# Performance work log

Measured on AMD Instinct MI355X. Metric: run time of the kernel, lower is better.

Reference implementation:

```python
import jax, jax.numpy as jnp
import numpy as np

BZ, QL, KL, D = 8, 2048, 2048, 128
SCALE = 1.0 / (D ** 0.5)
NEG = -1000000000.0


def setup_inputs() -> dict:
    key = jax.random.key(0)
    kq, kk, kv, km = jax.random.split(key, 4)
    q = jax.random.normal(kq, (BZ, QL, D), dtype=jnp.float32)
    k = jax.random.normal(kk, (BZ, KL, D), dtype=jnp.float32)
    v = jax.random.normal(kv, (BZ, KL, D), dtype=jnp.float32)
    mask = jax.random.randint(km, (BZ, KL), 0, 2).astype(jnp.bool_)
    return {"q": q, "k": k, "v": v, "mask": mask}


def reference(q, k, v, mask):
    # scores: (bz, q_len, k_len)
    score = jnp.einsum('bqd,bkd->bqk', q, k) * SCALE
    # masked_fill where ~mask (padding positions) with -1e9
    score = jnp.where(mask[:, None, :], score, NEG)
    weights = jax.nn.softmax(score, axis=-1)
    # (bz, q_len, v_dim)
    return jnp.einsum('bqk,bkd->bqd', weights, v)
```

## Files before the change

kernel.cpp:

```cpp
#include <hip/hip_runtime.h>
#include <hip/hip_bf16.h>


#define BZ 8
#define QL 2048
#define KLEN 2048
#define DH 128
#define NSL 64
#define SLICE_E 4096
#define PPITCH 40

typedef float f32x4 __attribute__((ext_vector_type(4)));
typedef int   i32x4 __attribute__((ext_vector_type(4)));
typedef __bf16 bf16x8 __attribute__((ext_vector_type(8)));
typedef __bf16 bf16x4 __attribute__((ext_vector_type(4)));
typedef __bf16 bf16x2 __attribute__((ext_vector_type(2)));

#define QSC 0.12751879523298232f
#define NEGV -1000000000.0f

__global__ void prep_kv(const float* __restrict__ kg, const float* __restrict__ vg,
                        __bf16* __restrict__ khat, __bf16* __restrict__ vhat) {
  const int blk = blockIdx.x;
  const int bs = blk & 511;
  const int b = bs & 7, s = bs >> 3;
  const int tid = threadIdx.x;
#pragma unroll
  for (int i = 0; i < 2; ++i) {
    const int c = i * 256 + tid;
    const int ln = c & 63, lc = ln & 15, qd = ln >> 4;
    if (blk < 512) {
      const int ff = (c >> 6) & 1, kf = c >> 7;
      const int key = s * 32 + ff * 16 + lc;
      const float* src = kg + ((size_t)(b * KLEN + key)) * DH + kf * 32 + qd * 8;
      f32x4 a = *(const f32x4*)src;
      f32x4 d = *(const f32x4*)(src + 4);
      bf16x8 w;
      w[0]=(__bf16)a[0]; w[1]=(__bf16)a[1]; w[2]=(__bf16)a[2]; w[3]=(__bf16)a[3];
      w[4]=(__bf16)d[0]; w[5]=(__bf16)d[1]; w[6]=(__bf16)d[2]; w[7]=(__bf16)d[3];
      *(bf16x8*)&khat[((size_t)(b * 64 + s) * 512 + c) * 8] = w;
    } else {
      const int nt = c >> 6;
      const float* src = vg + ((size_t)(b * KLEN + s * 32 + qd * 8)) * DH + nt * 16 + lc;
      bf16x8 w;
#pragma unroll
      for (int j = 0; j < 8; ++j) w[j] = (__bf16)src[(size_t)j * DH];
      *(bf16x8*)&vhat[((size_t)(b * 64 + s) * 512 + c) * 8] = w;
    }
  }
}

__global__ __launch_bounds__(512, 2) void fattn12(
    const __bf16* __restrict__ khat, const __bf16* __restrict__ vhat,
    const float* __restrict__ qg_, const int* __restrict__ maskg,
    float* __restrict__ outg) {
  __shared__ __align__(16) __bf16 sP[8][2][16 * PPITCH];
  __shared__ __align__(16) float fb[8192 + 64];

  const int tid = threadIdx.x;
  const int wv = tid >> 6, ln = tid & 63;
  const int qd = ln >> 4, lc = ln & 15;
  const int ab = blockIdx.x & 7, qt = blockIdx.x >> 3;
  const int q0 = qt * 64;
  const int qg = wv & 1, sl = wv >> 1;

  bf16x8 qf[2][4];
#pragma unroll
  for (int qp = 0; qp < 2; ++qp) {
    const float* qr = qg_ + ((size_t)(ab * QL + q0 + qg * 32 + qp * 16 + lc)) * DH + qd * 8;
#pragma unroll
    for (int kf = 0; kf < 4; ++kf) {
      f32x4 a = *(const f32x4*)(qr + kf * 32);
      f32x4 c = *(const f32x4*)(qr + kf * 32 + 4);
      bf16x8 t;
      t[0]=(__bf16)(a[0]*QSC); t[1]=(__bf16)(a[1]*QSC); t[2]=(__bf16)(a[2]*QSC); t[3]=(__bf16)(a[3]*QSC);
      t[4]=(__bf16)(c[0]*QSC); t[5]=(__bf16)(c[1]*QSC); t[6]=(__bf16)(c[2]*QSC); t[7]=(__bf16)(c[3]*QSC);
      qf[qp][kf] = t;
    }
  }

  const __bf16* Kb = khat + (size_t)ab * NSL * SLICE_E;
  const __bf16* Vb = vhat + (size_t)ab * NSL * SLICE_E;
  const int* mrow = maskg + ab * KLEN;
  __bf16* sp0 = &sP[wv][0][0];
  __bf16* sp1 = &sP[wv][1][0];

  f32x4 oacc[2][8];
#pragma unroll
  for (int qp = 0; qp < 2; ++qp)
#pragma unroll
    for (int i = 0; i < 8; ++i) oacc[qp][i] = (f32x4){0.f, 0.f, 0.f, 0.f};
  float li[2] = {0.f, 0.f};

  bf16x8 kA[4][2], kB[4][2], vA[8];
  bf16x8 pf0, pf1;
  i32x4 mA0, mA1, mB0, mB1;
  f32x4 sa[2][2];
  const int s0 = sl * 16;

  auto loadK = [&](bf16x8 (&dst)[4][2], int sidx) {
    const __bf16* ks = Kb + (size_t)sidx * SLICE_E;
#pragma unroll
    for (int kf = 0; kf < 4; ++kf)
#pragma unroll
      for (int f = 0; f < 2; ++f)
        dst[kf][f] = *(const bf16x8*)&ks[((kf * 2 + f) * 64 + ln) * 8];
  };
  auto loadM = [&](i32x4& m0, i32x4& m1, int sidx) {
    m0 = *(const i32x4*)&mrow[sidx * 32 + qd * 4];
    m1 = *(const i32x4*)&mrow[sidx * 32 + 16 + qd * 4];
  };
  auto loadV = [&](int sidx) {
    const __bf16* vs = Vb + (size_t)sidx * SLICE_E;
#pragma unroll
    for (int nt = 0; nt < 8; ++nt)
      vA[nt] = *(const bf16x8*)&vs[(nt * 64 + ln) * 8];
  };
  auto qk = [&](const bf16x8 (&kk)[4][2]) {
#pragma unroll
    for (int f = 0; f < 2; ++f)
#pragma unroll
      for (int qp = 0; qp < 2; ++qp) sa[f][qp] = (f32x4){0.f, 0.f, 0.f, 0.f};
#pragma unroll
    for (int kf = 0; kf < 4; ++kf)
#pragma unroll
      for (int f = 0; f < 2; ++f) {
        sa[f][0] = __builtin_amdgcn_mfma_f32_16x16x32_bf16(kk[kf][f], qf[0][kf], sa[f][0], 0, 0, 0);
        sa[f][1] = __builtin_amdgcn_mfma_f32_16x16x32_bf16(kk[kf][f], qf[1][kf], sa[f][1], 0, 0, 0);
      }
  };
  auto pv = [&]() {
#pragma unroll
    for (int nt = 0; nt < 8; ++nt) {
      oacc[0][nt] = __builtin_amdgcn_mfma_f32_16x16x32_bf16(vA[nt], pf0, oacc[0][nt], 0, 0, 0);
      oacc[1][nt] = __builtin_amdgcn_mfma_f32_16x16x32_bf16(vA[nt], pf1, oacc[1][nt], 0, 0, 0);
    }
  };
  auto softmax = [&](const i32x4& m0, const i32x4& m1) {
#pragma unroll
    for (int qp = 0; qp < 2; ++qp) {
      float ps[2][4];
#pragma unroll
      for (int r = 0; r < 4; ++r) {
        float p0 = __builtin_amdgcn_exp2f(sa[0][qp][r]);
        float p1 = __builtin_amdgcn_exp2f(sa[1][qp][r]);
        ps[0][r] = m0[r] ? p0 : 0.f;
        ps[1][r] = m1[r] ? p1 : 0.f;
      }
      li[qp] += ((ps[0][0] + ps[0][1]) + (ps[0][2] + ps[0][3])) +
                ((ps[1][0] + ps[1][1]) + (ps[1][2] + ps[1][3]));
      __bf16* sp = (qp == 0) ? sp0 : sp1;
#pragma unroll
      for (int f = 0; f < 2; ++f) {
        bf16x4 pw;
        pw[0] = (__bf16)ps[f][0]; pw[1] = (__bf16)ps[f][1];
        pw[2] = (__bf16)ps[f][2]; pw[3] = (__bf16)ps[f][3];
        *(bf16x4*)&sp[lc * PPITCH + f * 16 + qd * 4] = pw;
      }
    }
    pf0 = *(const bf16x8*)&sp0[lc * PPITCH + qd * 8];
    pf1 = *(const bf16x8*)&sp1[lc * PPITCH + qd * 8];
  };

  loadK(kA, s0);
  loadM(mA0, mA1, s0);
  loadK(kB, s0 + 1);
  loadM(mB0, mB1, s0 + 1);
  loadV(s0);
  qk(kA);
  softmax(mA0, mA1);

  for (int du = 0; du < 7; ++du) {
    {
      const int s = s0 + 2 * du + 1;
      __builtin_amdgcn_s_barrier();
      loadK(kA, s + 1);
      loadM(mA0, mA1, s + 1);
      __builtin_amdgcn_sched_barrier(0);
      __builtin_amdgcn_s_setprio(1);
      qk(kB);
      pv();
      __builtin_amdgcn_s_setprio(0);
      loadV(s);
      softmax(mB0, mB1);
    }
    {
      const int s = s0 + 2 * du + 2;
      __builtin_amdgcn_s_barrier();
      loadK(kB, s + 1);
      loadM(mB0, mB1, s + 1);
      __builtin_amdgcn_sched_barrier(0);
      __builtin_amdgcn_s_setprio(1);
      qk(kA);
      pv();
      __builtin_amdgcn_s_setprio(0);
      loadV(s);
      softmax(mA0, mA1);
    }
  }
  {
    const int s = s0 + 15;
    __builtin_amdgcn_s_barrier();
    __builtin_amdgcn_s_setprio(1);
    qk(kB);
    pv();
    __builtin_amdgcn_s_setprio(0);
    loadV(s);
    softmax(mB0, mB1);
  }
  pv();

#pragma unroll
  for (int qp = 0; qp < 2; ++qp) {
    li[qp] += __shfl_xor(li[qp], 16, 64);
    li[qp] += __shfl_xor(li[qp], 32, 64);
  }

  f32x4* mOv = (f32x4*)fb;
  float* sml = fb + 8192;
  auto publish = [&]() {
#pragma unroll
    for (int qp = 0; qp < 2; ++qp) {
#pragma unroll
      for (int nt = 0; nt < 8; ++nt)
        mOv[((qg * 2 + qp) * 8 + nt) * 64 + ln] = oacc[qp][nt];
      if (qd == 0) sml[(qg * 2 + qp) * 16 + lc] = li[qp];
    }
  };
  auto absorb = [&]() {
#pragma unroll
    for (int qp = 0; qp < 2; ++qp) {
      li[qp] += sml[(qg * 2 + qp) * 16 + lc];
#pragma unroll
      for (int nt = 0; nt < 8; ++nt) {
        f32x4 o2 = mOv[((qg * 2 + qp) * 8 + nt) * 64 + ln];
#pragma unroll
        for (int r = 0; r < 4; ++r) oacc[qp][nt][r] += o2[r];
      }
    }
  };

  __syncthreads();
  if (sl == 3) publish();
  __syncthreads();
  if (sl == 2) absorb();
  __syncthreads();
  if (sl == 1) publish();
  __syncthreads();
  if (sl == 0) absorb();
  __syncthreads();
  if (sl == 2) publish();
  __syncthreads();
  if (sl == 0) {
    absorb();
#pragma unroll
    for (int qp = 0; qp < 2; ++qp) {
      const float invL = 1.0f / li[qp];
      float* orow = outg + ((size_t)(ab * QL + q0 + qg * 32 + qp * 16 + lc)) * DH;
#pragma unroll
      for (int nt = 0; nt < 8; ++nt) {
        f32x4 res;
#pragma unroll
        for (int r = 0; r < 4; ++r) res[r] = oacc[qp][nt][r] * invL;
        *(f32x4*)&orow[nt * 16 + qd * 4] = res;
      }
    }
  }
}

#define KT 64
#define KPITCH 136
#define VPITCH 72
#define PPITCH2 72

__global__ __launch_bounds__(256, 1) void fattn_mono(
    const float* __restrict__ qgp, const float* __restrict__ kg,
    const float* __restrict__ vg, const int* __restrict__ maskg,
    float* __restrict__ outg) {
  __shared__ __bf16 sK[KT][KPITCH];
  __shared__ __bf16 sVT[DH][VPITCH];
  __shared__ __bf16 sPm[4][16][PPITCH2];

  const int tid = threadIdx.x;
  const int wv = tid >> 6, ln = tid & 63;
  const int qd = ln >> 4, lc = ln & 15;
  const int bid = blockIdx.x;
  const int b = bid >> 5;
  const int q0 = (bid & 31) << 6;
  const int qw = q0 + (wv << 4);

  bf16x8 qf[4];
  {
    const float* qr = qgp + ((size_t)(b * QL + qw + lc)) * DH + qd * 8;
#pragma unroll
    for (int kf = 0; kf < 4; ++kf) {
      f32x4 a = *(const f32x4*)(qr + kf * 32);
      f32x4 c = *(const f32x4*)(qr + kf * 32 + 4);
      bf16x8 t;
      t[0]=(__bf16)(a[0]*QSC); t[1]=(__bf16)(a[1]*QSC); t[2]=(__bf16)(a[2]*QSC); t[3]=(__bf16)(a[3]*QSC);
      t[4]=(__bf16)(c[0]*QSC); t[5]=(__bf16)(c[1]*QSC); t[6]=(__bf16)(c[2]*QSC); t[7]=(__bf16)(c[3]*QSC);
      qf[kf] = t;
    }
  }

  const float* kb = kg + (size_t)b * KLEN * DH;
  const float* vb = vg + (size_t)b * KLEN * DH;
  const int* mrow = maskg + b * KLEN;

  f32x4 kreg[8], va[4], vbr[4];

  auto load_tile = [&](int t) {
    const float* kt = kb + ((size_t)t * KT) * DH;
#pragma unroll
    for (int it = 0; it < 8; ++it) {
      int f = it * 256 + tid;
      kreg[it] = *(const f32x4*)(kt + (size_t)(f >> 5) * DH + (f & 31) * 4);
    }
    const float* vt = vb + ((size_t)t * KT) * DH;
#pragma unroll
    for (int it = 0; it < 4; ++it) {
      int u = it * 256 + tid;
      int m = u & 31, dc = (u >> 5) * 4;
      va[it]  = *(const f32x4*)(vt + (size_t)(2 * m) * DH + dc);
      vbr[it] = *(const f32x4*)(vt + (size_t)(2 * m + 1) * DH + dc);
    }
  };
  auto store_tile = [&]() {
#pragma unroll
    for (int it = 0; it < 8; ++it) {
      int f = it * 256 + tid;
      bf16x4 w;
      w[0]=(__bf16)kreg[it][0]; w[1]=(__bf16)kreg[it][1];
      w[2]=(__bf16)kreg[it][2]; w[3]=(__bf16)kreg[it][3];
      *(bf16x4*)&sK[f >> 5][(f & 31) * 4] = w;
    }
#pragma unroll
    for (int it = 0; it < 4; ++it) {
      int u = it * 256 + tid;
      int m = u & 31, dc = (u >> 5) * 4;
#pragma unroll
      for (int j = 0; j < 4; ++j) {
        bf16x2 p2;
        p2[0] = (__bf16)va[it][j];
        p2[1] = (__bf16)vbr[it][j];
        *(bf16x2*)&sVT[dc + j][2 * m] = p2;
      }
    }
  };

  f32x4 oacc[8];
#pragma unroll
  for (int i = 0; i < 8; ++i) oacc[i] = (f32x4){0.f, 0.f, 0.f, 0.f};
  float mi[4] = {-INFINITY, -INFINITY, -INFINITY, -INFINITY};
  float li[4] = {0.f, 0.f, 0.f, 0.f};

  load_tile(0); store_tile(); __syncthreads();

  for (int t = 0; t < (KLEN / KT); ++t) {
    const bool more = (t + 1 < (KLEN / KT));
    if (more) load_tile(t + 1);

    f32x4 sa[4];
#pragma unroll
    for (int f = 0; f < 4; ++f) sa[f] = (f32x4){0.f, 0.f, 0.f, 0.f};
#pragma unroll
    for (int kf = 0; kf < 4; ++kf)
#pragma unroll
      for (int f = 0; f < 4; ++f) {
        bf16x8 bk = *(const bf16x8*)&sK[f * 16 + lc][kf * 32 + qd * 8];
        sa[f] = __builtin_amdgcn_mfma_f32_16x16x32_bf16(qf[kf], bk, sa[f], 0, 0, 0);
      }

    const int kv0 = t * KT;
#pragma unroll
    for (int f = 0; f < 4; ++f) {
      const bool keep = mrow[kv0 + f * 16 + lc] != 0;
#pragma unroll
      for (int r = 0; r < 4; ++r) sa[f][r] = keep ? sa[f][r] : NEGV;
    }

    float rm[4], alpha[4], rs[4];
#pragma unroll
    for (int r = 0; r < 4; ++r)
      rm[r] = fmaxf(fmaxf(sa[0][r], sa[1][r]), fmaxf(sa[2][r], sa[3][r]));
#pragma unroll
    for (int sh = 0; sh < 4; ++sh) {
      const int off = 1 << sh;
#pragma unroll
      for (int r = 0; r < 4; ++r) rm[r] = fmaxf(rm[r], __shfl_xor(rm[r], off, 64));
    }
#pragma unroll
    for (int r = 0; r < 4; ++r) {
      float mn = fmaxf(mi[r], rm[r]);
      alpha[r] = __builtin_amdgcn_exp2f(mi[r] - mn);
      mi[r] = mn; rs[r] = 0.f;
    }
#pragma unroll
    for (int f = 0; f < 4; ++f)
#pragma unroll
      for (int r = 0; r < 4; ++r) {
        float p = __builtin_amdgcn_exp2f(sa[f][r] - mi[r]);
        sa[f][r] = p; rs[r] += p;
      }
#pragma unroll
    for (int sh = 0; sh < 4; ++sh) {
      const int off = 1 << sh;
#pragma unroll
      for (int r = 0; r < 4; ++r) rs[r] += __shfl_xor(rs[r], off, 64);
    }
#pragma unroll
    for (int r = 0; r < 4; ++r) li[r] = li[r] * alpha[r] + rs[r];

#pragma unroll
    for (int f = 0; f < 4; ++f)
#pragma unroll
      for (int r = 0; r < 4; ++r)
        sPm[wv][qd * 4 + r][f * 16 + lc] = (__bf16)sa[f][r];
#pragma unroll
    for (int nt = 0; nt < 8; ++nt)
#pragma unroll
      for (int r = 0; r < 4; ++r) oacc[nt][r] *= alpha[r];

#pragma unroll
    for (int kp = 0; kp < 2; ++kp) {
      bf16x8 ap = *(const bf16x8*)&sPm[wv][lc][kp * 32 + qd * 8];
#pragma unroll
      for (int nt = 0; nt < 8; ++nt) {
        bf16x8 bv = *(const bf16x8*)&sVT[nt * 16 + lc][kp * 32 + qd * 8];
        oacc[nt] = __builtin_amdgcn_mfma_f32_16x16x32_bf16(ap, bv, oacc[nt], 0, 0, 0);
      }
    }

    __syncthreads();
    if (more) store_tile();
    __syncthreads();
  }

  float inv[4];
#pragma unroll
  for (int r = 0; r < 4; ++r) inv[r] = 1.0f / li[r];
  float* orow = outg + ((size_t)(b * QL + qw)) * DH;
#pragma unroll
  for (int nt = 0; nt < 8; ++nt)
#pragma unroll
    for (int r = 0; r < 4; ++r)
      orow[(size_t)(qd * 4 + r) * DH + nt * 16 + lc] = oacc[nt][r] * inv[r];
}

extern "C" void kernel_launch(void* const* d_in, const int* in_sizes, int n_in,
                              void* d_out, int out_size, void* d_ws, size_t ws_size,
                              hipStream_t stream) {
  (void)in_sizes; (void)n_in; (void)out_size;
  const float* q = (const float*)d_in[0];
  const float* k = (const float*)d_in[1];
  const float* v = (const float*)d_in[2];
  const int* mask = (const int*)d_in[3];
  float* out = (float*)d_out;

  const size_t kv_elems = (size_t)BZ * KLEN * DH;
  if (ws_size >= 2 * kv_elems * sizeof(__bf16)) {
    __bf16* khat = (__bf16*)d_ws;
    __bf16* vhat = khat + kv_elems;
    prep_kv<<<dim3(1024), dim3(256), 0, stream>>>(k, v, khat, vhat);
    fattn12<<<dim3(256), dim3(512), 0, stream>>>(khat, vhat, q, mask, out);
  } else {
    fattn_mono<<<dim3(BZ * (QL / 64)), dim3(256), 0, stream>>>(q, k, v, mask, out);
  }
}
```

Baseline: 105.0 us.

## Drop per-iteration workgroup barriers and flatten cross-wave output reduction

```diff
diff --git a/kernel.cpp b/kernel.cpp
--- a/kernel.cpp
+++ b/kernel.cpp
@@ -50,12 +50,12 @@
   }
 }
 
-__global__ __launch_bounds__(512, 2) void fattn12(
+__global__ __launch_bounds__(512, 2) void fattn14(
     const __bf16* __restrict__ khat, const __bf16* __restrict__ vhat,
     const float* __restrict__ qg_, const int* __restrict__ maskg,
     float* __restrict__ outg) {
   __shared__ __align__(16) __bf16 sP[8][2][16 * PPITCH];
-  __shared__ __align__(16) float fb[8192 + 64];
+  __shared__ __align__(16) float fb[24576 + 192];
 
   const int tid = threadIdx.x;
   const int wv = tid >> 6, ln = tid & 63;
@@ -173,10 +173,8 @@
   for (int du = 0; du < 7; ++du) {
     {
       const int s = s0 + 2 * du + 1;
-      __builtin_amdgcn_s_barrier();
       loadK(kA, s + 1);
       loadM(mA0, mA1, s + 1);
-      __builtin_amdgcn_sched_barrier(0);
       __builtin_amdgcn_s_setprio(1);
       qk(kB);
       pv();
@@ -186,10 +184,8 @@
     }
     {
       const int s = s0 + 2 * du + 2;
-      __builtin_amdgcn_s_barrier();
       loadK(kB, s + 1);
       loadM(mB0, mB1, s + 1);
-      __builtin_amdgcn_sched_barrier(0);
       __builtin_amdgcn_s_setprio(1);
       qk(kA);
       pv();
@@ -200,7 +196,6 @@
   }
   {
     const int s = s0 + 15;
-    __builtin_amdgcn_s_barrier();
     __builtin_amdgcn_s_setprio(1);
     qk(kB);
     pv();
@@ -217,42 +212,32 @@
   }
 
   f32x4* mOv = (f32x4*)fb;
-  float* sml = fb + 8192;
-  auto publish = [&]() {
+  float* sml = fb + 24576;
+  if (sl != 0) {
+    const int m = sl - 1;
 #pragma unroll
     for (int qp = 0; qp < 2; ++qp) {
 #pragma unroll
       for (int nt = 0; nt < 8; ++nt)
-        mOv[((qg * 2 + qp) * 8 + nt) * 64 + ln] = oacc[qp][nt];
-      if (qd == 0) sml[(qg * 2 + qp) * 16 + lc] = li[qp];
-    }
-  };
-  auto absorb = [&]() {
-#pragma unroll
-    for (int qp = 0; qp < 2; ++qp) {
-      li[qp] += sml[(qg * 2 + qp) * 16 + lc];
-#pragma unroll
-      for (int nt = 0; nt < 8; ++nt) {
-        f32x4 o2 = mOv[((qg * 2 + qp) * 8 + nt) * 64 + ln];
-#pragma unroll
-        for (int r = 0; r < 4; ++r) oacc[qp][nt][r] += o2[r];
-      }
-    }
-  };
-
-  __syncthreads();
-  if (sl == 3) publish();
-  __syncthreads();
-  if (sl == 2) absorb();
-  __syncthreads();
-  if (sl == 1) publish();
-  __syncthreads();
-  if (sl == 0) absorb();
-  __syncthreads();
-  if (sl == 2) publish();
+        mOv[(((m * 2 + qp) * 2 + qg) * 8 + nt) * 64 + ln] = oacc[qp][nt];
+      if (qd == 0) sml[((m * 2 + qp) * 2 + qg) * 16 + lc] = li[qp];
+    }
+  }
   __syncthreads();
   if (sl == 0) {
-    absorb();
+#pragma unroll
+    for (int m = 0; m < 3; ++m) {
+#pragma unroll
+      for (int qp = 0; qp < 2; ++qp) {
+        li[qp] += sml[((m * 2 + qp) * 2 + qg) * 16 + lc];
+#pragma unroll
+        for (int nt = 0; nt < 8; ++nt) {
+          f32x4 o2 = mOv[(((m * 2 + qp) * 2 + qg) * 8 + nt) * 64 + ln];
+#pragma unroll
+          for (int r = 0; r < 4; ++r) oacc[qp][nt][r] += o2[r];
+        }
+      }
+    }
 #pragma unroll
     for (int qp = 0; qp < 2; ++qp) {
       const float invL = 1.0f / li[qp];
@@ -462,7 +447,7 @@
     __bf16* khat = (__bf16*)d_ws;
     __bf16* vhat = khat + kv_elems;
     prep_kv<<<dim3(1024), dim3(256), 0, stream>>>(k, v, khat, vhat);
-    fattn12<<<dim3(256), dim3(512), 0, stream>>>(khat, vhat, q, mask, out);
+    fattn14<<<dim3(256), dim3(512), 0, stream>>>(khat, vhat, q, mask, out);
   } else {
     fattn_mono<<<dim3(BZ * (QL / 64)), dim3(256), 0, stream>>>(q, k, v, mask, out);
   }
```

Result: no change. 103.3 us (-1.7%).
